# Kernel optimization log

Measured on AMD Instinct MI355X. Metric: run time of the kernel, lower is better.

The kernel has to match this reference:

```python
import jax, jax.numpy as jnp
import numpy as np

# dims: StyleGAN2 modulated conv at 64x64, 512 channels
B, IC, OC, K, SD, H, W = 16, 512, 512, 3, 512, 64, 64
EPS = 1e-8


def setup_inputs() -> dict:
    key = jax.random.key(0)
    k1, k2, k3, k4 = jax.random.split(key, 4)
    return {
        "input": jax.random.normal(k1, (B, IC, H, W), dtype=jnp.float32),
        "style": jax.random.normal(k2, (B, SD), dtype=jnp.float32),
        # learned params
        "weight": jax.random.normal(k3, (1, OC, IC, K, K), dtype=jnp.float32),
        "mod_weight": jax.random.normal(k4, (IC, SD), dtype=jnp.float32),
        "mod_bias": jnp.ones((IC,), dtype=jnp.float32),  # bias_init=1
    }


def reference(input, style, weight, mod_weight, mod_bias):
    conv_scale = 1.0 / np.sqrt(IC * K * K)   # 1/sqrt(fan_in)
    mod_scale = 1.0 / np.sqrt(SD)            # EqualLinear scale, lr_mul=1

    # style modulation: EqualLinear(style_dim -> in_channel), no activation
    s = style @ (mod_weight * mod_scale).T + mod_bias          # [B, IC]

    # per-sample modulated weight [B, OC, IC, K, K]
    w = conv_scale * weight * s[:, None, :, None, None]
    # demodulation over (in_channel, kh, kw)
    demod = jax.lax.rsqrt(jnp.sum(w * w, axis=(2, 3, 4)) + EPS)  # [B, OC]
    w = w * demod[:, :, None, None, None]

    # grouped conv with groups=batch (same trick as torch F.conv2d groups=B)
    x = input.reshape(1, B * IC, H, W)
    wg = w.reshape(B * OC, IC, K, K)
    pad = K // 2
    out = jax.lax.conv_general_dilated(
        x, wg,
        window_strides=(1, 1),
        padding=[(pad, pad), (pad, pad)],
        dimension_numbers=("NCHW", "OIHW", "NCHW"),
        feature_group_count=B,
    )
    return out.reshape(B, OC, H, W)
```

## Files before the change

### kernel.cpp

```cpp
#include <hip/hip_runtime.h>
#include <hip/hip_bf16.h>

constexpr int BB = 16, IC = 512, OC = 512, HH = 64, WW = 64, HW = 64 * 64, SD = 512;
constexpr float MOD_SCALE = 0.04419417382415922f;
constexpr float CONV_SCALE = 0.014731391274719739f;
constexpr float CONV_SCALE2 = 2.170138888888889e-4f;

typedef float f32x4 __attribute__((ext_vector_type(4)));
typedef short bf16x8 __attribute__((ext_vector_type(8)));

#define VMWAIT(n) asm volatile("s_waitcnt vmcnt(" #n ")" ::: "memory")
#define LGKM0()   asm volatile("s_waitcnt lgkmcnt(0)" ::: "memory")

__device__ __forceinline__ unsigned short f2bf(float x) {
  __hip_bfloat16 h = __float2bfloat16(x);
  return *(unsigned short*)&h;
}

__global__ void k_style(const float* __restrict__ style, const float* __restrict__ mw,
                        const float* __restrict__ mb, float* __restrict__ s) {
  __shared__ float st[SD];
  const int b = blockIdx.x;
  for (int i = threadIdx.x; i < SD; i += 256) st[i] = style[b * SD + i];
  __syncthreads();
  for (int ic = threadIdx.x; ic < IC; ic += 256) {
    const float4* wr = (const float4*)(mw + (size_t)ic * SD);
    float acc = 0.f;
    for (int d = 0; d < SD / 4; ++d) {
      float4 w4 = wr[d];
      float4 s4 = *(const float4*)&st[d * 4];
      acc += w4.x * s4.x + w4.y * s4.y + w4.z * s4.z + w4.w * s4.w;
    }
    s[b * IC + ic] = acc * MOD_SCALE + mb[ic];
  }
}

__global__ void k_pack(const float* __restrict__ w, unsigned short* __restrict__ wpack,
                       float* __restrict__ w2sum) {
  const int oc = blockIdx.x;
  const int ic0 = threadIdx.x * 2;
  const float* p = w + (size_t)oc * IC * 9 + (size_t)ic0 * 9;
  float v[18];
#pragma unroll
  for (int i = 0; i < 18; ++i) v[i] = p[i];
  float s0 = 0.f, s1 = 0.f;
#pragma unroll
  for (int t = 0; t < 9; ++t) { s0 += v[t] * v[t]; s1 += v[9 + t] * v[9 + t]; }
  *(float2*)&w2sum[oc * IC + ic0] = make_float2(s0, s1);
#pragma unroll
  for (int t = 0; t < 9; ++t) {
    unsigned int pk = (unsigned int)f2bf(v[t]) | ((unsigned int)f2bf(v[9 + t]) << 16);
    *(unsigned int*)&wpack[((size_t)t * OC + oc) * IC + ic0] = pk;
  }
}

__global__ void k_demod(const float* __restrict__ s, const float* __restrict__ w2sum,
                        float* __restrict__ fscale) {
  __shared__ float s2[IC];
  const int b = blockIdx.x;
  for (int i = threadIdx.x; i < IC; i += 256) { float v = s[b * IC + i]; s2[i] = v * v; }
  __syncthreads();
  for (int oc = threadIdx.x; oc < OC; oc += 256) {
    const float4* wr = (const float4*)(w2sum + (size_t)oc * IC);
    float acc = 0.f;
    for (int i4 = 0; i4 < IC / 4; ++i4) {
      float4 w4 = wr[i4];
      float4 q4 = *(const float4*)&s2[i4 * 4];
      acc += w4.x * q4.x + w4.y * q4.y + w4.z * q4.z + w4.w * q4.w;
    }
    fscale[b * OC + oc] = CONV_SCALE * rsqrtf(CONV_SCALE2 * acc + 1e-8f);
  }
}

#define RD_AF(DST, NB)                                                         \
  do {                                                                         \
    _Pragma("unroll") for (int i_ = 0; i_ < 4; ++i_) {                         \
      int r_ = i_ * 16 + lrow;                                                 \
      DST[i_] = *(const bf16x8*)&Apool[wm][(NB)][r_ * 32 +                     \
                                               ((lk ^ ((r_ >> 1) & 3)) * 8)];  \
    }                                                                          \
  } while (0)

#define RD_BF(DST, TN, BI)                                                     \
  do {                                                                         \
    const int dh_ = (TN) / 3 - 1, dw_ = (TN) % 3 - 1;                          \
    _Pragma("unroll") for (int j_ = 0; j_ < 4; ++j_) {                         \
      int r_ = (wn + dh_ + 1) * 66 + j_ * 16 + lrow + dw_ + 1;                 \
      DST[j_] = *(const bf16x8*)&Bsm[(BI)][r_ * 32 +                           \
                                          ((lk ^ ((r_ >> 1) & 3)) * 8)];       \
    }                                                                          \
  } while (0)

#define MFMA16(AF, BF)                                                         \
  do {                                                                         \
    _Pragma("unroll") for (int i_ = 0; i_ < 4; ++i_)                           \
      _Pragma("unroll") for (int j_ = 0; j_ < 4; ++j_)                         \
        acc[i_][j_] = __builtin_amdgcn_mfma_f32_16x16x32_bf16(AF[i_], BF[j_],  \
                                                              acc[i_][j_], 0, 0, 0); \
  } while (0)

__global__ __launch_bounds__(256, 2) void k_conv(
    const float* __restrict__ x, const unsigned short* __restrict__ wpack,
    const float* __restrict__ s, const float* __restrict__ fscale,
    float* __restrict__ out) {
  __shared__ __align__(128) unsigned short Apool[2][3][64 * 32];
  __shared__ __align__(128) unsigned short Bsm[2][264 * 32];

  const int bx = ((blockIdx.x & 7) << 8) | (blockIdx.x >> 3);
  const int b = bx >> 7, mblk = (bx >> 5) & 3, nblk = bx & 31;

  const int tid = threadIdx.x;
  const int wave = tid >> 6, lane = tid & 63;
  const int wm = wave >> 1, wn = wave & 1;
  const int lrow = lane & 15, lk = lane >> 4;
  const int h0 = nblk * 2;

  const float* xb = x + (size_t)b * IC * HW;
  const float* sb = s + b * IC;

  f32x4 acc[4][4];
#pragma unroll
  for (int i = 0; i < 4; ++i)
#pragma unroll
    for (int j = 0; j < 4; ++j) acc[i][j] = f32x4{0.f, 0.f, 0.f, 0.f};

#pragma unroll
  for (int z = 0; z < 2; ++z) {
    int q = (tid >> 5) + z * 8;
    int bi = q >> 3;
    int hh = (q >> 1) & 3, wz = (q & 1) ? 65 : 0;
    Bsm[bi][(hh * 66 + wz) * 32 + (tid & 31)] = 0;
  }

  auto stageB = [&](int icb, int bi) {
    const int hh = wave;
    const int h_abs = h0 - 1 + hh;
    const bool vh = (h_abs >= 0) && (h_abs < HH);
    const int h_safe = vh ? h_abs : 0;
    const int r = hh * 66 + lane + 1;
    const int swz = (r >> 1) & 3;
    const float* src = xb + (size_t)(icb * 32) * HW + h_safe * WW + lane;
#pragma unroll
    for (int c = 0; c < 4; ++c) {
      unsigned int pk[4];
#pragma unroll
      for (int jj = 0; jj < 4; ++jj) {
        int ic = c * 8 + jj * 2;
        float m0 = vh ? sb[icb * 32 + ic] : 0.f;
        float m1 = vh ? sb[icb * 32 + ic + 1] : 0.f;
        pk[jj] = (unsigned int)f2bf(src[(size_t)ic * HW] * m0) |
                 ((unsigned int)f2bf(src[(size_t)(ic + 1) * HW] * m1) << 16);
      }
      *(uint4*)&Bsm[bi][r * 32 + ((c ^ swz) * 8)] = make_uint4(pk[0], pk[1], pk[2], pk[3]);
    }
  };

  auto issueA = [&](int tap, int icb, int nb) {
    const unsigned short* base =
        wpack + ((size_t)(tap * OC + mblk * 128 + wm * 64)) * IC + icb * 32;
    unsigned short* dst = &Apool[wm][nb][0];
#pragma unroll
    for (int q = 0; q < 4; ++q) {
      int rl = q * 16 + (lane >> 2);
      int cs = (lane & 3) ^ ((rl >> 1) & 3);
      const unsigned short* g = base + (size_t)rl * IC + cs * 8;
      __builtin_amdgcn_global_load_lds(
          (const __attribute__((address_space(1))) void*)g,
          (__attribute__((address_space(3))) void*)(dst + q * 16 * 32), 16, 0, 0);
    }
  };

  stageB(0, 0);
  issueA(0, 0, 0);
  issueA(1, 0, 1);
  __syncthreads();

  bf16x8 afA[4], afB[4], bfA[4], bfB[4];
  RD_AF(afA, 0);
  RD_BF(bfA, 0, 0);

  for (int e = 0; e < 16; e += 2) {
#pragma unroll
    for (int tt = 0; tt < 18; ++tt) {
      const int t = tt % 9;
      const int io = tt / 9;
      const int icb = e + io;
      const bool last = (e == 14) && (io == 1);
      const int P = (io + t) & 1;

      __builtin_amdgcn_s_barrier();
      __builtin_amdgcn_sched_barrier(0);

      __builtin_amdgcn_s_setprio(1);
      if (P == 0) { MFMA16(afA, bfA); } else { MFMA16(afB, bfB); }
      __builtin_amdgcn_s_setprio(0);
      __builtin_amdgcn_sched_barrier(0);

      if (!(last && t >= 7)) {
        if (t <= 6) issueA(t + 2, icb, (t + 2) % 3);
        else        issueA(t - 7, icb + 1, (t + 2) % 3);
      }

      if (!(last && t == 8)) {
        if (last && t == 7) { VMWAIT(0); } else { VMWAIT(4); }
        __builtin_amdgcn_sched_barrier(0);
        if (P == 0) {
          RD_AF(afB, (t + 1) % 3);
          if (t < 8) { RD_BF(bfB, t + 1, io); }
          else       { RD_BF(bfB, 0, 1 - io); }
        } else {
          RD_AF(afA, (t + 1) % 3);
          if (t < 8) { RD_BF(bfA, t + 1, io); }
          else       { RD_BF(bfA, 0, 1 - io); }
        }
      }

      if (t == 4 && !(e == 14 && io == 1)) {
        stageB(icb + 1, 1 - io);
        LGKM0();
        __builtin_amdgcn_sched_barrier(0);
      }
    }
  }

  const float* fsb = fscale + b * OC;
#pragma unroll
  for (int i = 0; i < 4; ++i) {
#pragma unroll
    for (int rr = 0; rr < 4; ++rr) {
      const int oc = mblk * 128 + wm * 64 + i * 16 + lk * 4 + rr;
      const float sc = fsb[oc];
      float* orow = out + ((size_t)(b * OC + oc)) * HW + nblk * 128 + wn * 64 + lrow;
#pragma unroll
      for (int j = 0; j < 4; ++j) orow[j * 16] = acc[i][j][rr] * sc;
    }
  }
}

extern "C" void kernel_launch(void* const* d_in, const int* in_sizes, int n_in,
                              void* d_out, int out_size, void* d_ws, size_t ws_size,
                              hipStream_t stream) {
  const float* input = (const float*)d_in[0];
  const float* style = (const float*)d_in[1];
  const float* weight = (const float*)d_in[2];
  const float* mod_weight = (const float*)d_in[3];
  const float* mod_bias = (const float*)d_in[4];
  float* out = (float*)d_out;

  char* ws = (char*)d_ws;
  constexpr size_t WPACK_B = (size_t)9 * OC * IC * 2;
  constexpr size_t W2SUM_B = (size_t)OC * IC * 4;
  constexpr size_t S_B = (size_t)BB * IC * 4;
  unsigned short* wpack = (unsigned short*)ws;
  float* w2sum = (float*)(ws + WPACK_B);
  float* s = (float*)(ws + WPACK_B + W2SUM_B);
  float* fscale = (float*)(ws + WPACK_B + W2SUM_B + S_B);

  k_style<<<BB, 256, 0, stream>>>(style, mod_weight, mod_bias, s);
  k_pack<<<OC, 256, 0, stream>>>(weight, wpack, w2sum);
  k_demod<<<BB, 256, 0, stream>>>(s, w2sum, fscale);
  k_conv<<<2048, 256, 0, stream>>>(input, wpack, s, fscale, out);
}
```

Measured before the change: 473.7 us.

## Load weight fragments straight to registers and widen conv blocks to 8 waves

Drops the LDS staging of the packed weight tile, which was filled with global_load_lds. Each wave now loads its MFMA A fragments directly from global memory into registers, one tap ahead. The conv block grows to 512 threads covering 256 output channels, so each input tile is staged into LDS half as often, and the staging work is split over 8 waves. Workgroup barriers now fire every third tap instead of every tap. The risk is that global-load latency on the A operand is only hidden by a single tap of prefetch and has no explicit wait control, and the bigger blocks may lower occupancy.

```diff
diff --git a/kernel.cpp b/kernel.cpp
--- a/kernel.cpp
+++ b/kernel.cpp
@@ -9,7 +9,6 @@
 typedef float f32x4 __attribute__((ext_vector_type(4)));
 typedef short bf16x8 __attribute__((ext_vector_type(8)));
 
-#define VMWAIT(n) asm volatile("s_waitcnt vmcnt(" #n ")" ::: "memory")
 #define LGKM0()   asm volatile("s_waitcnt lgkmcnt(0)" ::: "memory")
 
 __device__ __forceinline__ unsigned short f2bf(float x) {
@@ -72,12 +71,11 @@
   }
 }
 
-#define RD_AF(DST, NB)                                                         \
+#define LD_AF(DST, TN, ICB)                                                    \
   do {                                                                         \
     _Pragma("unroll") for (int i_ = 0; i_ < 4; ++i_) {                         \
-      int r_ = i_ * 16 + lrow;                                                 \
-      DST[i_] = *(const bf16x8*)&Apool[wm][(NB)][r_ * 32 +                     \
-                                               ((lk ^ ((r_ >> 1) & 3)) * 8)];  \
+      DST[i_] = *(const bf16x8*)(wpA + ((size_t)(TN)*OC + i_ * 16) * IC +      \
+                                 (size_t)(ICB) * 32);                          \
     }                                                                          \
   } while (0)
 
@@ -99,15 +97,14 @@
                                                               acc[i_][j_], 0, 0, 0); \
   } while (0)
 
-__global__ __launch_bounds__(256, 2) void k_conv(
+__global__ __launch_bounds__(512, 2) void k_conv(
     const float* __restrict__ x, const unsigned short* __restrict__ wpack,
     const float* __restrict__ s, const float* __restrict__ fscale,
     float* __restrict__ out) {
-  __shared__ __align__(128) unsigned short Apool[2][3][64 * 32];
   __shared__ __align__(128) unsigned short Bsm[2][264 * 32];
 
-  const int bx = ((blockIdx.x & 7) << 8) | (blockIdx.x >> 3);
-  const int b = bx >> 7, mblk = (bx >> 5) & 3, nblk = bx & 31;
+  const int bx = ((blockIdx.x & 7) << 7) | (blockIdx.x >> 3);
+  const int b = bx >> 6, mblk = (bx >> 5) & 1, nblk = bx & 31;
 
   const int tid = threadIdx.x;
   const int wave = tid >> 6, lane = tid & 63;
@@ -118,22 +115,24 @@
   const float* xb = x + (size_t)b * IC * HW;
   const float* sb = s + b * IC;
 
+  const unsigned short* wpA =
+      wpack + ((size_t)(mblk * 256 + wm * 64 + lrow)) * IC + lk * 8;
+
   f32x4 acc[4][4];
 #pragma unroll
   for (int i = 0; i < 4; ++i)
 #pragma unroll
     for (int j = 0; j < 4; ++j) acc[i][j] = f32x4{0.f, 0.f, 0.f, 0.f};
 
-#pragma unroll
-  for (int z = 0; z < 2; ++z) {
-    int q = (tid >> 5) + z * 8;
+  {
+    int q = tid >> 5;
     int bi = q >> 3;
     int hh = (q >> 1) & 3, wz = (q & 1) ? 65 : 0;
     Bsm[bi][(hh * 66 + wz) * 32 + (tid & 31)] = 0;
   }
 
   auto stageB = [&](int icb, int bi) {
-    const int hh = wave;
+    const int hh = wave & 3;
     const int h_abs = h0 - 1 + hh;
     const bool vh = (h_abs >= 0) && (h_abs < HH);
     const int h_safe = vh ? h_abs : 0;
@@ -141,7 +140,8 @@
     const int swz = (r >> 1) & 3;
     const float* src = xb + (size_t)(icb * 32) * HW + h_safe * WW + lane;
 #pragma unroll
-    for (int c = 0; c < 4; ++c) {
+    for (int cc = 0; cc < 2; ++cc) {
+      const int c = (wave >> 2) * 2 + cc;
       unsigned int pk[4];
 #pragma unroll
       for (int jj = 0; jj < 4; ++jj) {
@@ -151,32 +151,15 @@
         pk[jj] = (unsigned int)f2bf(src[(size_t)ic * HW] * m0) |
                  ((unsigned int)f2bf(src[(size_t)(ic + 1) * HW] * m1) << 16);
       }
-      *(uint4*)&Bsm[bi][r * 32 + ((c ^ swz) * 8)] = make_uint4(pk[0], pk[1], pk[2], pk[3]);
+      *(uint4*)&Bsm[bi][r * 32 + ((c ^ swz) * 8)] =
+          make_uint4(pk[0], pk[1], pk[2], pk[3]);
     }
   };
 
-  auto issueA = [&](int tap, int icb, int nb) {
-    const unsigned short* base =
-        wpack + ((size_t)(tap * OC + mblk * 128 + wm * 64)) * IC + icb * 32;
-    unsigned short* dst = &Apool[wm][nb][0];
-#pragma unroll
-    for (int q = 0; q < 4; ++q) {
-      int rl = q * 16 + (lane >> 2);
-      int cs = (lane & 3) ^ ((rl >> 1) & 3);
-      const unsigned short* g = base + (size_t)rl * IC + cs * 8;
-      __builtin_amdgcn_global_load_lds(
-          (const __attribute__((address_space(1))) void*)g,
-          (__attribute__((address_space(3))) void*)(dst + q * 16 * 32), 16, 0, 0);
-    }
-  };
-
   stageB(0, 0);
-  issueA(0, 0, 0);
-  issueA(1, 0, 1);
+  bf16x8 afA[4], afB[4], bfA[4], bfB[4];
+  LD_AF(afA, 0, 0);
   __syncthreads();
-
-  bf16x8 afA[4], afB[4], bfA[4], bfB[4];
-  RD_AF(afA, 0);
   RD_BF(bfA, 0, 0);
 
   for (int e = 0; e < 16; e += 2) {
@@ -188,30 +171,29 @@
       const bool last = (e == 14) && (io == 1);
       const int P = (io + t) & 1;
 
-      __builtin_amdgcn_s_barrier();
-      __builtin_amdgcn_sched_barrier(0);
+      if (t % 3 == 0) {
+        __builtin_amdgcn_s_barrier();
+        __builtin_amdgcn_sched_barrier(0);
+      }
+
+      if (!(last && t == 8)) {
+        if (P == 0) {
+          if (t < 8) { LD_AF(afB, t + 1, icb); } else { LD_AF(afB, 0, icb + 1); }
+        } else {
+          if (t < 8) { LD_AF(afA, t + 1, icb); } else { LD_AF(afA, 0, icb + 1); }
+        }
+      }
 
       __builtin_amdgcn_s_setprio(1);
       if (P == 0) { MFMA16(afA, bfA); } else { MFMA16(afB, bfB); }
       __builtin_amdgcn_s_setprio(0);
       __builtin_amdgcn_sched_barrier(0);
 
-      if (!(last && t >= 7)) {
-        if (t <= 6) issueA(t + 2, icb, (t + 2) % 3);
-        else        issueA(t - 7, icb + 1, (t + 2) % 3);
-      }
-
       if (!(last && t == 8)) {
-        if (last && t == 7) { VMWAIT(0); } else { VMWAIT(4); }
-        __builtin_amdgcn_sched_barrier(0);
         if (P == 0) {
-          RD_AF(afB, (t + 1) % 3);
-          if (t < 8) { RD_BF(bfB, t + 1, io); }
-          else       { RD_BF(bfB, 0, 1 - io); }
+          if (t < 8) { RD_BF(bfB, t + 1, io); } else { RD_BF(bfB, 0, 1 - io); }
         } else {
-          RD_AF(afA, (t + 1) % 3);
-          if (t < 8) { RD_BF(bfA, t + 1, io); }
-          else       { RD_BF(bfA, 0, 1 - io); }
+          if (t < 8) { RD_BF(bfA, t + 1, io); } else { RD_BF(bfA, 0, 1 - io); }
         }
       }
 
@@ -228,7 +210,7 @@
   for (int i = 0; i < 4; ++i) {
 #pragma unroll
     for (int rr = 0; rr < 4; ++rr) {
-      const int oc = mblk * 128 + wm * 64 + i * 16 + lk * 4 + rr;
+      const int oc = mblk * 256 + wm * 64 + i * 16 + lk * 4 + rr;
       const float sc = fsb[oc];
       float* orow = out + ((size_t)(b * OC + oc)) * HW + nblk * 128 + wn * 64 + lrow;
 #pragma unroll
@@ -259,5 +241,5 @@
   k_style<<<BB, 256, 0, stream>>>(style, mod_weight, mod_bias, s);
   k_pack<<<OC, 256, 0, stream>>>(weight, wpack, w2sum);
   k_demod<<<BB, 256, 0, stream>>>(s, w2sum, fscale);
-  k_conv<<<2048, 256, 0, stream>>>(input, wpack, s, fscale, out);
-}
+  k_conv<<<1024, 512, 0, stream>>>(input, wpack, s, fscale, out);
+}
```

Result: slower. 665.8 us (+40.6%).
